# Kernel tuning notes

Hardware: AMD Instinct MI355X
Metric: run time of the kernel (lower is better)

Reference implementation:

```python
import jax, jax.numpy as jnp
import numpy as np

# dims
B, L, HID = 2, 1024, 2048
NH, HD, NKV = 32, 64, 8
INTER = 8192
DSSM, MH, MP, MS, MG, MK = 2048, 32, 64, 64, 1, 4
CONV_DIM = DSSM + 2 * MG * MS
EPS = 1e-5
ROPE_BASE = 1e11
# multipliers from config
KEY_MULT, ATTN_IN, ATTN_OUT = 0.7, 1.2, 0.8
SSM_IN, SSM_OUT = 1.1, 0.9
GATE_MULT, DOWN_MULT = 0.9, 0.8
SSM_MULTS = (1.0, 0.9, 0.8, 1.1, 1.2)


def _rms(x, w, eps=EPS):
    return x * jax.lax.rsqrt(jnp.mean(x * x, -1, keepdims=True) + eps) * w


def _rope(pos, x):  # neox-style, full head_dim; x: (B,L,H,HD)
    half = HD // 2
    inv = ROPE_BASE ** (-jnp.arange(0, HD, 2, dtype=jnp.float32) / HD)
    ang = pos.astype(jnp.float32)[:, None] * inv  # (L, half)
    cos = jnp.cos(ang)[None, :, None, :]
    sin = jnp.sin(ang)[None, :, None, :]
    x1, x2 = x[..., :half], x[..., half:]
    return jnp.concatenate([x1 * cos - x2 * sin, x2 * cos + x1 * sin], -1)


def _mup_vector():
    return jnp.concatenate([
        jnp.full((DSSM,), SSM_MULTS[0], jnp.float32),
        jnp.full((DSSM,), SSM_MULTS[1], jnp.float32),
        jnp.full((MG * MS,), SSM_MULTS[2], jnp.float32),
        jnp.full((MG * MS,), SSM_MULTS[3], jnp.float32),
        jnp.full((MH,), SSM_MULTS[4], jnp.float32),
    ])


def setup_inputs() -> dict:
    key = jax.random.key(0)
    ks = jax.random.split(key, 16)
    s = 0.02
    return {
        "hidden_states": jax.random.normal(ks[0], (B, L, HID), jnp.float32),
        "positions": jnp.arange(L, dtype=jnp.int32),
        "w_in_ln": jnp.ones((HID,), jnp.float32),
        "qkv_w": jax.random.normal(ks[1], (NH * HD + 2 * NKV * HD, HID), jnp.float32) * s,
        "o_w": jax.random.normal(ks[2], (HID, NH * HD), jnp.float32) * s,
        "in_proj_w": jax.random.normal(ks[3], (2 * DSSM + 2 * MG * MS + MH, HID), jnp.float32) * s,
        "conv_w": jax.random.normal(ks[4], (CONV_DIM, MK), jnp.float32) * 0.1,
        "conv_b": jax.random.normal(ks[5], (CONV_DIM,), jnp.float32) * 0.01,
        "A_log": jnp.log(jnp.linspace(1.0, 16.0, MH, dtype=jnp.float32)),
        "dt_bias": jax.random.normal(ks[6], (MH,), jnp.float32) * 0.1,
        "D": jnp.ones((MH,), jnp.float32),
        "ssm_norm_w": jnp.ones((DSSM,), jnp.float32),
        "out_proj_w": jax.random.normal(ks[7], (HID, DSSM), jnp.float32) * s,
        "w_pre_ff_ln": jnp.ones((HID,), jnp.float32),
        "gate_up_w": jax.random.normal(ks[8], (2 * INTER, HID), jnp.float32) * s,
        "down_w": jax.random.normal(ks[9], (HID, INTER), jnp.float32) * s,
    }


def _attention(hs, positions, qkv_w, o_w):
    qkv = hs @ qkv_w.T
    qs, kvs = NH * HD, NKV * HD
    q = qkv[..., :qs].reshape(B, L, NH, HD)
    k = qkv[..., qs:qs + kvs].reshape(B, L, NKV, HD) * KEY_MULT
    v = qkv[..., qs + kvs:].reshape(B, L, NKV, HD)
    q = _rope(positions, q)
    k = _rope(positions, k)
    rep = NH // NKV
    qg = q.reshape(B, L, NKV, rep, HD)
    scores = jnp.einsum('blgrd,bmgd->bgrlm', qg, k) * (HD ** -0.5)
    mask = jnp.tril(jnp.ones((L, L), bool))
    scores = jnp.where(mask[None, None, None], scores, jnp.float32(-1e9))
    attn = jax.nn.softmax(scores, axis=-1)
    out = jnp.einsum('bgrlm,bmgd->blgrd', attn, v).reshape(B, L, NH * HD)
    return out @ o_w.T


def _mamba(hs, in_proj_w, conv_w, conv_b, A_log, dt_bias, D, ssm_norm_w, out_proj_w):
    proj = (hs @ in_proj_w.T) * _mup_vector()  # (B,L,2*DSSM+2*G*S+MH)
    z = proj[..., :DSSM]
    xBC = proj[..., DSSM:DSSM + CONV_DIM]
    dt = proj[..., -MH:]
    # causal depthwise conv1d, kernel MK, then silu
    xpad = jnp.pad(xBC, ((0, 0), (MK - 1, 0), (0, 0)))
    conv = sum(xpad[:, k:k + L, :] * conv_w[:, k] for k in range(MK)) + conv_b
    xBC = jax.nn.silu(conv)
    x = xBC[..., :DSSM].reshape(B, L, MH, MP)
    Bm = xBC[..., DSSM:DSSM + MG * MS].reshape(B, L, MS)  # G=1
    C = xBC[..., DSSM + MG * MS:].reshape(B, L, MS)
    dt = jax.nn.softplus(dt + dt_bias)  # (B,L,MH)
    A = -jnp.exp(A_log)  # (MH,)

    def step(state, inp):  # state: (B,MH,MP,MS)
        x_t, dt_t, b_t, c_t = inp  # (B,MH,MP),(B,MH),(B,MS),(B,MS)
        dA = jnp.exp(dt_t * A)  # (B,MH)
        dBx = dt_t[..., None, None] * x_t[..., None] * b_t[:, None, None, :]
        state = state * dA[..., None, None] + dBx
        y = jnp.einsum('bhps,bs->bhp', state, c_t)
        return state, y

    xs = (jnp.moveaxis(x, 1, 0), jnp.moveaxis(dt, 1, 0),
          jnp.moveaxis(Bm, 1, 0), jnp.moveaxis(C, 1, 0))
    state0 = jnp.zeros((B, MH, MP, MS), hs.dtype)
    _, ys = jax.lax.scan(step, state0, xs)
    y = jnp.moveaxis(ys, 0, 1) + x * D[None, None, :, None]  # (B,L,MH,MP)
    y = y.reshape(B, L, DSSM)
    # gated RMSNorm: gate with silu(z), then rms-normalize
    g = y * jax.nn.silu(z)
    g = _rms(g, ssm_norm_w)
    return g @ out_proj_w.T


def _mlp(x, gate_up_w, down_w):
    gu = x @ gate_up_w.T
    gate = gu[..., :INTER] * GATE_MULT
    up = gu[..., INTER:]
    return (jax.nn.silu(gate) * up) @ down_w.T * DOWN_MULT


def reference(hidden_states, positions, w_in_ln, qkv_w, o_w, in_proj_w, conv_w,
              conv_b, A_log, dt_bias, D, ssm_norm_w, out_proj_w, w_pre_ff_ln,
              gate_up_w, down_w):
    residual = hidden_states
    hs = _rms(hidden_states, w_in_ln)
    attn_h = _attention(hs * ATTN_IN, positions, qkv_w, o_w)
    ssm_h = _mamba(hs * SSM_IN, in_proj_w, conv_w, conv_b, A_log, dt_bias, D,
                   ssm_norm_w, out_proj_w)
    h = attn_h * ATTN_OUT + ssm_h * SSM_OUT + residual
    residual = h
    h = _rms(h, w_pre_ff_ln)
    h = _mlp(h, gate_up_w, down_w)
    return h + residual
```

## Files before the change

### kernel.cpp

```cpp
#include <hip/hip_runtime.h>
#include <hip/hip_bf16.h>
#include <math.h>

#define B_      2
#define L_      1024
#define HID     2048
#define T_      (B_*L_)
#define NH      32
#define HD      64
#define NKV     8
#define INTER   8192
#define DSSM    2048
#define MH      32
#define MP      64
#define MS      64
#define MK      4
#define CONV_DIM 2176
#define QKV_N   3072
#define INPROJ_N 4256
#define CH      16
#define CL      64

typedef __bf16 bf16x8 __attribute__((ext_vector_type(8)));
typedef __bf16 bf16x4 __attribute__((ext_vector_type(4)));
typedef float  floatx4 __attribute__((ext_vector_type(4)));

static const size_t OFF_H2   = 0;
static const size_t OFF_MUP  = 4194304;
static const size_t AR       = 4210688;
static const size_t OFF_WQKV = AR;
static const size_t OFF_WIN  = OFF_WQKV + 3145728;
static const size_t OFF_WO   = OFF_WIN  + 4358144;
static const size_t OFF_WOP  = OFF_WO   + 2097152;
static const size_t OFF_HSB  = OFF_WOP  + 2097152;
static const size_t OFF_HSF  = OFF_HSB  + 2097152;
static const size_t OFF_QKV  = OFF_HSF  + 4194304;
static const size_t OFF_Q    = OFF_QKV  + 6291456;
static const size_t OFF_K    = OFF_Q    + 2097152;
static const size_t OFF_V    = OFF_K    + 524288;
static const size_t OFF_ATT  = OFF_V    + 524288;
static const size_t OFF_PROJ = OFF_ATT  + 2097152;
static const size_t OFF_XBC  = OFF_PROJ + 8716288;
static const size_t OFF_Y    = OFF_XBC  + 4456448;
static const size_t OFF_G    = OFF_Y    + 4194304;
static const size_t OFF_TB   = OFF_QKV;
static const size_t OFF_DEC  = OFF_Q;
static const size_t OFF_LAM  = OFF_V;
static const size_t OFF_HS2B = AR;
static const size_t OFF_GU   = AR + 2097152;
static const size_t OFF_ACTB = OFF_GU + 33554432;
static const size_t OFF_WB2  = OFF_ACTB + 8388608;

__device__ inline float block_sum(float v, float* red) {
#pragma unroll
  for (int o = 32; o > 0; o >>= 1) v += __shfl_down(v, o, 64);
  const int lane = threadIdx.x & 63, wv = threadIdx.x >> 6;
  if (lane == 0) red[wv] = v;
  __syncthreads();
  if (threadIdx.x == 0) red[0] = red[0] + red[1] + red[2] + red[3];
  __syncthreads();
  float r = red[0];
  __syncthreads();
  return r;
}

__device__ inline bf16x8 pack8(float4 a, float4 b, float scale) {
  bf16x8 v;
  v[0] = (__bf16)(a.x * scale); v[1] = (__bf16)(a.y * scale);
  v[2] = (__bf16)(a.z * scale); v[3] = (__bf16)(a.w * scale);
  v[4] = (__bf16)(b.x * scale); v[5] = (__bf16)(b.y * scale);
  v[6] = (__bf16)(b.z * scale); v[7] = (__bf16)(b.w * scale);
  return v;
}

__device__ __forceinline__ void async16(const void* g, void* l) {
  __builtin_amdgcn_global_load_lds(
      (const __attribute__((address_space(1))) void*)g,
      (__attribute__((address_space(3))) void*)l, 16, 0, 0);
}

__global__ __launch_bounds__(256) void cvt_kernel(
    const float* __restrict__ in, __bf16* __restrict__ outp, int n8)
{
  int i = blockIdx.x * 256 + threadIdx.x;
  const int stride = gridDim.x * 256;
  for (; i < n8; i += stride) {
    const float4* p = (const float4*)(in + (size_t)i * 8);
    float4 a = p[0], b = p[1];
    bf16x8 v;
    v[0] = (__bf16)a.x; v[1] = (__bf16)a.y; v[2] = (__bf16)a.z; v[3] = (__bf16)a.w;
    v[4] = (__bf16)b.x; v[5] = (__bf16)b.y; v[6] = (__bf16)b.z; v[7] = (__bf16)b.w;
    *(bf16x8*)(outp + (size_t)i * 8) = v;
  }
}

__global__ __launch_bounds__(256) void copy_kernel(
    const float* __restrict__ in, float* __restrict__ outp)
{
  const size_t i = ((size_t)blockIdx.x * 256 + threadIdx.x) * 4;
  *(float4*)&outp[i] = *(const float4*)&in[i];
}

__global__ __launch_bounds__(256) void gemm_bf_kernel(
    const __bf16* __restrict__ A, const __bf16* __restrict__ W,
    float* __restrict__ out, const float* __restrict__ addin,
    const float* __restrict__ colscale,
    int N, int K, int ldo, float alpha)
{
  __shared__ __align__(16) __bf16 As[2][128 * 32];
  __shared__ __align__(16) __bf16 Bs[2][128 * 32];
  const int tid = threadIdx.x;
  const int lane = tid & 63, wave = tid >> 6;
  const int fr = lane & 15, fq = lane >> 4;

  const int nwg = (int)(gridDim.x * gridDim.y);
  int lid = (int)(blockIdx.y * gridDim.x + blockIdx.x);
  lid = (lid & 7) * (nwg >> 3) + (lid >> 3);
  const int m0 = (lid & 15) * 128;
  const int n0 = (lid >> 4) * 128;
  const int wm = (wave >> 1) * 64, wn = (wave & 1) * 64;

  const int KS = K / gridDim.z;
  const int kbase = (int)blockIdx.z * KS;

  const int srow = wave * 32 + (lane >> 2);
  const int selem = (lane & 3) * 8;
  const __bf16* ga0 = A + (size_t)(m0 + srow) * K + kbase + selem;
  const __bf16* ga1 = ga0 + (size_t)16 * K;
  int wr0 = n0 + srow;      if (wr0 >= N) wr0 = N - 1;
  int wr1 = n0 + srow + 16; if (wr1 >= N) wr1 = N - 1;
  const __bf16* gb0 = W + (size_t)wr0 * K + kbase + selem;
  const __bf16* gb1 = W + (size_t)wr1 * K + kbase + selem;
  const int sbase = wave * 2 * 512;

  floatx4 acc[4][4];
#pragma unroll
  for (int i = 0; i < 4; i++)
#pragma unroll
    for (int j = 0; j < 4; j++) acc[i][j] = (floatx4){0.f, 0.f, 0.f, 0.f};

  async16(ga0, &As[0][sbase]); async16(ga1, &As[0][sbase + 512]);
  async16(gb0, &Bs[0][sbase]); async16(gb1, &Bs[0][sbase + 512]);
  ga0 += 32; ga1 += 32; gb0 += 32; gb1 += 32;
  __syncthreads();

  const int nsteps = KS >> 5;
  int cur = 0;
  for (int s = 0; s < nsteps - 1; ++s) {
    async16(ga0, &As[cur ^ 1][sbase]); async16(ga1, &As[cur ^ 1][sbase + 512]);
    async16(gb0, &Bs[cur ^ 1][sbase]); async16(gb1, &Bs[cur ^ 1][sbase + 512]);
    ga0 += 32; ga1 += 32; gb0 += 32; gb1 += 32;

    bf16x8 aF[4], bF[4];
#pragma unroll
    for (int i = 0; i < 4; i++)
      aF[i] = *(const bf16x8*)&As[cur][(wm + i * 16 + fr) * 32 + fq * 8];
#pragma unroll
    for (int j = 0; j < 4; j++)
      bF[j] = *(const bf16x8*)&Bs[cur][(wn + j * 16 + fr) * 32 + fq * 8];
#pragma unroll
    for (int i = 0; i < 4; i++)
#pragma unroll
      for (int j = 0; j < 4; j++)
        acc[i][j] = __builtin_amdgcn_mfma_f32_16x16x32_bf16(aF[i], bF[j], acc[i][j], 0, 0, 0);

    __syncthreads();
    cur ^= 1;
  }

  {
    bf16x8 aF[4], bF[4];
#pragma unroll
    for (int i = 0; i < 4; i++)
      aF[i] = *(const bf16x8*)&As[cur][(wm + i * 16 + fr) * 32 + fq * 8];
#pragma unroll
    for (int j = 0; j < 4; j++)
      bF[j] = *(const bf16x8*)&Bs[cur][(wn + j * 16 + fr) * 32 + fq * 8];
#pragma unroll
    for (int i = 0; i < 4; i++)
#pragma unroll
      for (int j = 0; j < 4; j++)
        acc[i][j] = __builtin_amdgcn_mfma_f32_16x16x32_bf16(aF[i], bF[j], acc[i][j], 0, 0, 0);
  }

  const bool at = (gridDim.z > 1);
#pragma unroll
  for (int i = 0; i < 4; i++) {
#pragma unroll
    for (int r = 0; r < 4; r++) {
      const int m = m0 + wm + i * 16 + fq * 4 + r;
      float* orow = out + (size_t)m * ldo;
      const float* arow = addin ? (addin + (size_t)m * ldo) : nullptr;
#pragma unroll
      for (int j = 0; j < 4; j++) {
        const int n = n0 + wn + j * 16 + fr;
        if (n < N) {
          float vv = acc[i][j][r] * alpha;
          if (colscale) vv *= colscale[n];
          if (at) {
            atomicAdd(&orow[n], vv);
          } else {
            if (arow) vv += arow[n];
            orow[n] = vv;
          }
        }
      }
    }
  }
}

__global__ __launch_bounds__(256) void rms_kernel(
    const float* __restrict__ in, const float* __restrict__ w,
    __bf16* __restrict__ outb, float* __restrict__ outf, float* __restrict__ copy)
{
  __shared__ float buf[HID];
  __shared__ float red[8];
  const int tid = threadIdx.x;
  const size_t t = blockIdx.x;
  const float* row = in + t * HID;
  float ss = 0.f;
  for (int i = tid; i < HID; i += 256) { float x = row[i]; buf[i] = x; ss += x * x; }
  float tot = block_sum(ss, red);
  float inv = rsqrtf(tot / (float)HID + 1e-5f);
  for (int i = tid; i < HID; i += 256) {
    float x = buf[i];
    float val = x * inv * w[i];
    outb[t * HID + i] = (__bf16)val;
    if (outf) outf[t * HID + i] = val;
    if (copy) copy[t * HID + i] = x;
  }
}

__global__ void mup_kernel(float* __restrict__ mup) {
  int i = blockIdx.x * 256 + threadIdx.x;
  if (i >= INPROJ_N) return;
  float v = (i < DSSM) ? 1.0f
          : (i < 2 * DSSM) ? 0.9f
          : (i < 2 * DSSM + MS) ? 0.8f
          : (i < 2 * DSSM + 2 * MS) ? 1.1f
          : 1.2f;
  mup[i] = v;
}

__global__ __launch_bounds__(256) void rope_kernel(
    const float* __restrict__ qkv, const int* __restrict__ positions,
    __bf16* __restrict__ q, __bf16* __restrict__ k, __bf16* __restrict__ v)
{
  __shared__ float inv_s[32];
  const int tid = threadIdx.x;
  const size_t t = blockIdx.x;
  const int l = (int)(t & (L_ - 1));
  if (tid < 32) inv_s[tid] = powf(1.0e11f, -(float)(2 * tid) / 64.f);
  __syncthreads();
  const float pos = (float)positions[l];
  const float* src = qkv + t * QKV_N;
  for (int idx = tid; idx < 1536; idx += 256) {
    int head = idx >> 5, hd = idx & 31;
    if (head < 32) {
      float ang = pos * inv_s[hd];
      float c = cosf(ang), sn = sinf(ang);
      float x1 = src[head * 64 + hd], x2 = src[head * 64 + 32 + hd];
      __bf16* dst = q + (t * NH + head) * HD;
      dst[hd] = (__bf16)((x1 * c - x2 * sn) * 0.125f);
      dst[hd + 32] = (__bf16)((x2 * c + x1 * sn) * 0.125f);
    } else if (head < 40) {
      int kk = head - 32;
      float ang = pos * inv_s[hd];
      float c = cosf(ang), sn = sinf(ang);
      float x1 = src[2048 + kk * 64 + hd] * 0.7f;
      float x2 = src[2048 + kk * 64 + 32 + hd] * 0.7f;
      __bf16* dst = k + (t * NKV + kk) * HD;
      dst[hd] = (__bf16)(x1 * c - x2 * sn);
      dst[hd + 32] = (__bf16)(x2 * c + x1 * sn);
    } else {
      int vv = head - 40;
      __bf16* dst = v + (t * NKV + vv) * HD;
      dst[hd] = (__bf16)src[2560 + vv * 64 + hd];
      dst[hd + 32] = (__bf16)src[2560 + vv * 64 + 32 + hd];
    }
  }
}

__global__ __launch_bounds__(256) void fattn_kernel(
    const __bf16* __restrict__ q, const __bf16* __restrict__ k,
    const __bf16* __restrict__ v, __bf16* __restrict__ out)
{
  __shared__ __align__(16) __bf16 Vt[64][72];
  __shared__ __align__(16) __bf16 Ps[4][16][72];
  const int tid = threadIdx.x;
  const int wave = tid >> 6, lane = tid & 63;
  const int fr = lane & 15, fq = lane >> 4;
  const int qt = (int)(gridDim.x - 1) - blockIdx.x;
  const int h = blockIdx.y, b = blockIdx.z, g = h >> 2;
  const int l0 = qt * 64;

  bf16x8 qf[2];
  {
    const int qrow = l0 + wave * 16 + fr;
    const __bf16* qp = q + (((size_t)(b * L_ + qrow)) * NH + h) * HD;
    qf[0] = *(const bf16x8*)&qp[fq * 8];
    qf[1] = *(const bf16x8*)&qp[32 + fq * 8];
  }

  floatx4 O[4];
  float m_run[4], l_run[4];
#pragma unroll
  for (int i = 0; i < 4; i++) { O[i] = (floatx4){0.f,0.f,0.f,0.f}; m_run[i] = -3.0e38f; l_run[i] = 0.f; }

  for (int kt = 0; kt <= qt; kt++) {
    __syncthreads();
#pragma unroll
    for (int pp = 0; pp < 4; pp++) {
      const int kb = pp * 4 + wave;
      bf16x4 pk;
#pragma unroll
      for (int c = 0; c < 4; c++)
        pk[c] = v[(((size_t)(b * L_ + kt * 64 + kb * 4 + c)) * NKV + g) * HD + lane];
      *(bf16x4*)&Vt[lane][kb * 4] = pk;
    }

    floatx4 S[4];
#pragma unroll
    for (int j = 0; j < 4; j++) {
      const __bf16* kp = k + (((size_t)(b * L_ + kt * 64 + j * 16 + fr)) * NKV + g) * HD;
      floatx4 sa = (floatx4){0.f,0.f,0.f,0.f};
#pragma unroll
      for (int s = 0; s < 2; s++) {
        bf16x8 kf = *(const bf16x8*)&kp[s * 32 + fq * 8];
        sa = __builtin_amdgcn_mfma_f32_16x16x32_bf16(qf[s], kf, sa, 0, 0, 0);
      }
      S[j] = sa;
    }

    if (kt == qt) {
      const int qbase = wave * 16 + fq * 4;
#pragma unroll
      for (int j = 0; j < 4; j++)
#pragma unroll
        for (int r = 0; r < 4; r++)
          if (j * 16 + fr > qbase + r) S[j][r] = -1.0e30f;
    }

    float rm[4], alpha[4], rsum[4];
#pragma unroll
    for (int r = 0; r < 4; r++)
      rm[r] = fmaxf(fmaxf(S[0][r], S[1][r]), fmaxf(S[2][r], S[3][r]));
#pragma unroll
    for (int msk = 1; msk <= 8; msk <<= 1)
#pragma unroll
      for (int r = 0; r < 4; r++) rm[r] = fmaxf(rm[r], __shfl_xor(rm[r], msk, 64));
#pragma unroll
    for (int r = 0; r < 4; r++) {
      float mnew = fmaxf(m_run[r], rm[r]);
      alpha[r] = __expf(m_run[r] - mnew);
      m_run[r] = mnew;
    }
#pragma unroll
    for (int j = 0; j < 4; j++)
#pragma unroll
      for (int r = 0; r < 4; r++) S[j][r] = __expf(S[j][r] - m_run[r]);
#pragma unroll
    for (int r = 0; r < 4; r++)
      rsum[r] = S[0][r] + S[1][r] + S[2][r] + S[3][r];
#pragma unroll
    for (int msk = 1; msk <= 8; msk <<= 1)
#pragma unroll
      for (int r = 0; r < 4; r++) rsum[r] += __shfl_xor(rsum[r], msk, 64);
#pragma unroll
    for (int r = 0; r < 4; r++) l_run[r] = l_run[r] * alpha[r] + rsum[r];
#pragma unroll
    for (int d4 = 0; d4 < 4; d4++)
#pragma unroll
      for (int r = 0; r < 4; r++) O[d4][r] *= alpha[r];

#pragma unroll
    for (int j = 0; j < 4; j++)
#pragma unroll
      for (int r = 0; r < 4; r++)
        Ps[wave][fq * 4 + r][j * 16 + fr] = (__bf16)S[j][r];

    __syncthreads();

#pragma unroll
    for (int s = 0; s < 2; s++) {
      bf16x8 pf = *(const bf16x8*)&Ps[wave][fr][s * 32 + fq * 8];
#pragma unroll
      for (int d4 = 0; d4 < 4; d4++) {
        bf16x8 vf = *(const bf16x8*)&Vt[d4 * 16 + fr][s * 32 + fq * 8];
        O[d4] = __builtin_amdgcn_mfma_f32_16x16x32_bf16(pf, vf, O[d4], 0, 0, 0);
      }
    }
  }

  float rl[4];
#pragma unroll
  for (int r = 0; r < 4; r++) rl[r] = 1.f / l_run[r];
#pragma unroll
  for (int d4 = 0; d4 < 4; d4++)
#pragma unroll
    for (int r = 0; r < 4; r++) {
      const int qg = l0 + wave * 16 + fq * 4 + r;
      out[((size_t)(b * L_ + qg)) * HID + h * 64 + d4 * 16 + fr] = (__bf16)(O[d4][r] * rl[r]);
    }
}

__global__ __launch_bounds__(256) void dtfix_kernel(
    const float* __restrict__ hs_ln, const float* __restrict__ w, float* __restrict__ proj)
{
  const size_t t = blockIdx.x;
  const int tid = threadIdx.x;
  const int o = tid >> 3, part = tid & 7;
  const float* a = hs_ln + t * HID;
  const float* wr = w + (size_t)(INPROJ_N - MH + o) * HID;
  float s = 0.f;
  for (int kk = part * 4; kk < HID; kk += 32) {
    const float4 av = *(const float4*)&a[kk];
    const float4 wv = *(const float4*)&wr[kk];
    s += av.x * wv.x + av.y * wv.y + av.z * wv.z + av.w * wv.w;
  }
  s += __shfl_xor(s, 1);
  s += __shfl_xor(s, 2);
  s += __shfl_xor(s, 4);
  if (part == 0) proj[t * INPROJ_N + (INPROJ_N - MH) + o] = s * 1.32f;
}

__global__ __launch_bounds__(256) void conv_kernel(
    const float* __restrict__ proj, const float* __restrict__ cw,
    const float* __restrict__ cb, float* __restrict__ xbc)
{
  const int c = blockIdx.x * 256 + threadIdx.x;
  if (c >= CONV_DIM) return;
  const int t = blockIdx.y;
  const int l = t & (L_ - 1);
  float acc = cb[c];
#pragma unroll
  for (int kk = 0; kk < MK; kk++) {
    int lp = l - (MK - 1) + kk;
    if (lp >= 0)
      acc += proj[((size_t)(t - (MK - 1) + kk)) * INPROJ_N + DSSM + c] * cw[c * MK + kk];
  }
  xbc[(size_t)t * CONV_DIM + c] = acc / (1.f + __expf(-acc));
}

__global__ __launch_bounds__(256) void scanA_kernel(
    const float* __restrict__ xbc, const float* __restrict__ proj,
    const float* __restrict__ A_log, const float* __restrict__ dt_bias,
    const float* __restrict__ Dp,
    float* __restrict__ y, float* __restrict__ Tbuf,
    float* __restrict__ lam, float* __restrict__ dec)
{
  __shared__ __align__(16) __bf16 xT[64][72];
  __shared__ __align__(16) __bf16 BTw[64][72];
  __shared__ __align__(16) __bf16 Braw[64][72];
  __shared__ __align__(16) __bf16 Craw[64][72];
  __shared__ __align__(16) __bf16 Ps[4][16][72];
  __shared__ float dt_s[64], cum_s[64];

  const int tid = threadIdx.x;
  const int lane = tid & 63, wave = tid >> 6;
  const int fr = lane & 15, fq = lane >> 4;
  const int c = blockIdx.x, h = blockIdx.y, b = blockIdx.z;
  const int t0 = b * L_ + c * CL;
  const float Ah = -expf(A_log[h]);
  const float dtb = dt_bias[h], Dh = Dp[h];

  if (wave == 0) {
    float draw = proj[(size_t)(t0 + lane) * INPROJ_N + (INPROJ_N - MH) + h];
    float dtv = draw + dtb;
    dtv = (dtv > 20.f) ? dtv : log1pf(__expf(dtv));
    float cs = dtv * Ah;
#pragma unroll
    for (int d = 1; d < 64; d <<= 1) {
      float nv = __shfl_up(cs, d, 64);
      if (lane >= d) cs += nv;
    }
    dt_s[lane] = dtv;
    cum_s[lane] = cs;
  }

#pragma unroll
  for (int pass = 0; pass < 4; pass++) {
    const int l = pass * 16 + (tid >> 4);
    const int s4 = (tid & 15) * 4;
    const float* rowp = xbc + (size_t)(t0 + l) * CONV_DIM;
    float4 xv = *(const float4*)&rowp[h * 64 + s4];
    float4 bv = *(const float4*)&rowp[DSSM + s4];
    float4 cv = *(const float4*)&rowp[DSSM + MS + s4];
    xT[s4 + 0][l] = (__bf16)xv.x;
    xT[s4 + 1][l] = (__bf16)xv.y;
    xT[s4 + 2][l] = (__bf16)xv.z;
    xT[s4 + 3][l] = (__bf16)xv.w;
    bf16x4 b4; b4[0]=(__bf16)bv.x; b4[1]=(__bf16)bv.y; b4[2]=(__bf16)bv.z; b4[3]=(__bf16)bv.w;
    *(bf16x4*)&Braw[l][s4] = b4;
    bf16x4 c4; c4[0]=(__bf16)cv.x; c4[1]=(__bf16)cv.y; c4[2]=(__bf16)cv.z; c4[3]=(__bf16)cv.w;
    *(bf16x4*)&Craw[l][s4] = c4;
  }
  __syncthreads();

  const float cend = cum_s[63];
#pragma unroll
  for (int pass = 0; pass < 4; pass++) {
    const int l = pass * 16 + (tid >> 4);
    const int s4 = (tid & 15) * 4;
    const float wl = __expf(cend - cum_s[l]) * dt_s[l];
    float4 bv = *(const float4*)&xbc[(size_t)(t0 + l) * CONV_DIM + DSSM + s4];
    BTw[s4 + 0][l] = (__bf16)(bv.x * wl);
    BTw[s4 + 1][l] = (__bf16)(bv.y * wl);
    BTw[s4 + 2][l] = (__bf16)(bv.z * wl);
    BTw[s4 + 3][l] = (__bf16)(bv.w * wl);
  }

  {
    bf16x8 aF0 = *(const bf16x8*)&Craw[wave * 16 + fr][fq * 8];
    bf16x8 aF1 = *(const bf16x8*)&Craw[wave * 16 + fr][fq * 8 + 32];
#pragma unroll
    for (int j = 0; j < 4; j++) {
      floatx4 s = (floatx4){0.f,0.f,0.f,0.f};
      bf16x8 b0 = *(const bf16x8*)&Braw[j * 16 + fr][fq * 8];
      bf16x8 b1 = *(const bf16x8*)&Braw[j * 16 + fr][fq * 8 + 32];
      s = __builtin_amdgcn_mfma_f32_16x16x32_bf16(aF0, b0, s, 0, 0, 0);
      s = __builtin_amdgcn_mfma_f32_16x16x32_bf16(aF1, b1, s, 0, 0, 0);
      const int m = j * 16 + fr;
      const float dtm = dt_s[m], cmm = cum_s[m];
#pragma unroll
      for (int r = 0; r < 4; r++) {
        const int lR = wave * 16 + fq * 4 + r;
        float f = (m <= lR) ? __expf(cum_s[lR] - cmm) * dtm : 0.f;
        Ps[wave][fq * 4 + r][m] = (__bf16)(s[r] * f);
      }
    }
  }
  __syncthreads();

  {
    bf16x8 aF0 = *(const bf16x8*)&Ps[wave][fr][fq * 8];
    bf16x8 aF1 = *(const bf16x8*)&Ps[wave][fr][fq * 8 + 32];
#pragma unroll
    for (int j = 0; j < 4; j++) {
      floatx4 s = (floatx4){0.f,0.f,0.f,0.f};
      bf16x8 b0 = *(const bf16x8*)&xT[j * 16 + fr][fq * 8];
      bf16x8 b1 = *(const bf16x8*)&xT[j * 16 + fr][fq * 8 + 32];
      s = __builtin_amdgcn_mfma_f32_16x16x32_bf16(aF0, b0, s, 0, 0, 0);
      s = __builtin_amdgcn_mfma_f32_16x16x32_bf16(aF1, b1, s, 0, 0, 0);
      const int p = j * 16 + fr;
#pragma unroll
      for (int r = 0; r < 4; r++) {
        const int lR = wave * 16 + fq * 4 + r;
        float xval = (float)xT[p][lR];
        y[(size_t)(t0 + lR) * DSSM + h * 64 + p] = s[r] + Dh * xval;
      }
    }
  }

  {
    float* Tb = Tbuf + ((size_t)((b * MH + h) * CH + c)) * 4096;
    bf16x8 aF0 = *(const bf16x8*)&xT[wave * 16 + fr][fq * 8];
    bf16x8 aF1 = *(const bf16x8*)&xT[wave * 16 + fr][fq * 8 + 32];
#pragma unroll
    for (int j = 0; j < 4; j++) {
      floatx4 s = (floatx4){0.f,0.f,0.f,0.f};
      bf16x8 b0 = *(const bf16x8*)&BTw[j * 16 + fr][fq * 8];
      bf16x8 b1 = *(const bf16x8*)&BTw[j * 16 + fr][fq * 8 + 32];
      s = __builtin_amdgcn_mfma_f32_16x16x32_bf16(aF0, b0, s, 0, 0, 0);
      s = __builtin_amdgcn_mfma_f32_16x16x32_bf16(aF1, b1, s, 0, 0, 0);
#pragma unroll
      for (int r = 0; r < 4; r++)
        Tb[(wave * 16 + fq * 4 + r) * 64 + j * 16 + fr] = s[r];
    }
  }

  if (tid == 0) lam[(b * MH + h) * CH + c] = __expf(cend);
  if (tid >= 64 && tid < 128)
    dec[((size_t)((b * MH + h) * CH + c)) * 64 + (tid - 64)] = __expf(cum_s[tid - 64]);
}

__global__ __launch_bounds__(256) void scanB_kernel(
    const float* __restrict__ xbc, const float* __restrict__ Tbuf,
    const float* __restrict__ lam, const float* __restrict__ dec,
    float* __restrict__ y)
{
  __shared__ __align__(16) float S[64][68];
  __shared__ __align__(16) __bf16 Cc[64][72];
  __shared__ float decl[64];
  const int tid = threadIdx.x;
  const int lane = tid & 63, wave = tid >> 6;
  const int fr = lane & 15, fq = lane >> 4;
  const int h = blockIdx.x, b = blockIdx.y;

  const int sown = tid & 63, pbase = (tid >> 6) * 16;
#pragma unroll
  for (int i = 0; i < 16; i++) S[pbase + i][sown] = 0.f;
  __syncthreads();

  for (int c = 0; c < CH; c++) {
    const int t0 = b * L_ + c * CL;
#pragma unroll
    for (int pass = 0; pass < 4; pass++) {
      const int l = pass * 16 + (tid >> 4);
      const int s4 = (tid & 15) * 4;
      float4 cv = *(const float4*)&xbc[(size_t)(t0 + l) * CONV_DIM + DSSM + MS + s4];
      bf16x4 c4; c4[0]=(__bf16)cv.x; c4[1]=(__bf16)cv.y; c4[2]=(__bf16)cv.z; c4[3]=(__bf16)cv.w;
      *(bf16x4*)&Cc[l][s4] = c4;
    }
    if (tid < 64) decl[tid] = dec[((size_t)((b * MH + h) * CH + c)) * 64 + tid];
    __syncthreads();

    if (c > 0) {
      bf16x8 aF0 = *(const bf16x8*)&Cc[wave * 16 + fr][fq * 8];
      bf16x8 aF1 = *(const bf16x8*)&Cc[wave * 16 + fr][fq * 8 + 32];
#pragma unroll
      for (int j = 0; j < 4; j++) {
        const float* srow = &S[j * 16 + fr][0];
        float4 s0 = *(const float4*)&srow[fq * 8];
        float4 s1 = *(const float4*)&srow[fq * 8 + 4];
        float4 s2 = *(const float4*)&srow[fq * 8 + 32];
        float4 s3 = *(const float4*)&srow[fq * 8 + 36];
        bf16x8 b0 = pack8(s0, s1, 1.f);
        bf16x8 b1 = pack8(s2, s3, 1.f);
        floatx4 acc = (floatx4){0.f,0.f,0.f,0.f};
        acc = __builtin_amdgcn_mfma_f32_16x16x32_bf16(aF0, b0, acc, 0, 0, 0);
        acc = __builtin_amdgcn_mfma_f32_16x16x32_bf16(aF1, b1, acc, 0, 0, 0);
        const int p = j * 16 + fr;
#pragma unroll
        for (int r = 0; r < 4; r++) {
          const int lR = wave * 16 + fq * 4 + r;
          float* yp = &y[(size_t)(t0 + lR) * DSSM + h * 64 + p];
          *yp += decl[lR] * acc[r];
        }
      }
    }
    __syncthreads();

    const float lc = lam[(b * MH + h) * CH + c];
    const float* Tb = Tbuf + ((size_t)((b * MH + h) * CH + c)) * 4096;
#pragma unroll
    for (int i = 0; i < 16; i++) {
      float tv = Tb[(pbase + i) * 64 + sown];
      S[pbase + i][sown] = lc * S[pbase + i][sown] + tv;
    }
    __syncthreads();
  }
}

__global__ __launch_bounds__(256) void gating_kernel(
    const float* __restrict__ y, const float* __restrict__ proj,
    const float* __restrict__ nw, __bf16* __restrict__ g)
{
  __shared__ float buf[DSSM];
  __shared__ float red[8];
  const int tid = threadIdx.x;
  const size_t t = blockIdx.x;
  float ss = 0.f;
  for (int i = tid; i < DSSM; i += 256) {
    float zv = proj[t * INPROJ_N + i];
    float yv = y[t * DSSM + i];
    float gv = yv * zv / (1.f + __expf(-zv));
    buf[i] = gv;
    ss += gv * gv;
  }
  float tot = block_sum(ss, red);
  float inv = rsqrtf(tot / (float)DSSM + 1e-5f);
  for (int i = tid; i < DSSM; i += 256) g[t * DSSM + i] = (__bf16)(buf[i] * inv * nw[i]);
}

__global__ __launch_bounds__(256) void act_kernel(
    const float* __restrict__ gu, __bf16* __restrict__ act)
{
  const int i = (blockIdx.x * 256 + threadIdx.x) * 4;
  const size_t t = blockIdx.y;
  float4 g4 = *(const float4*)&gu[t * (2 * INTER) + i];
  float4 u4 = *(const float4*)&gu[t * (2 * INTER) + INTER + i];
  bf16x4 o;
  float gt;
  gt = g4.x * 0.9f; o[0] = (__bf16)(gt / (1.f + __expf(-gt)) * u4.x);
  gt = g4.y * 0.9f; o[1] = (__bf16)(gt / (1.f + __expf(-gt)) * u4.y);
  gt = g4.z * 0.9f; o[2] = (__bf16)(gt / (1.f + __expf(-gt)) * u4.z);
  gt = g4.w * 0.9f; o[3] = (__bf16)(gt / (1.f + __expf(-gt)) * u4.w);
  *(bf16x4*)&act[t * INTER + i] = o;
}

extern "C" void kernel_launch(void* const* d_in, const int* in_sizes, int n_in,
                              void* d_out, int out_size, void* d_ws, size_t ws_size,
                              hipStream_t stream)
{
  const float* hidden      = (const float*)d_in[0];
  const int*   positions   = (const int*)d_in[1];
  const float* w_in_ln     = (const float*)d_in[2];
  const float* qkv_w       = (const float*)d_in[3];
  const float* o_w         = (const float*)d_in[4];
  const float* in_proj_w   = (const float*)d_in[5];
  const float* conv_w      = (const float*)d_in[6];
  const float* conv_b      = (const float*)d_in[7];
  const float* A_log       = (const float*)d_in[8];
  const float* dt_bias     = (const float*)d_in[9];
  const float* Dp          = (const float*)d_in[10];
  const float* ssm_norm_w  = (const float*)d_in[11];
  const float* out_proj_w  = (const float*)d_in[12];
  const float* w_pre_ff_ln = (const float*)d_in[13];
  const float* gate_up_w   = (const float*)d_in[14];
  const float* down_w      = (const float*)d_in[15];
  (void)in_sizes; (void)n_in; (void)out_size; (void)ws_size;

  float* ws   = (float*)d_ws;
  float* outp = (float*)d_out;

  float*  h2    = ws + OFF_H2;
  float*  mup   = ws + OFF_MUP;
  __bf16* wqkv  = (__bf16*)(ws + OFF_WQKV);
  __bf16* win   = (__bf16*)(ws + OFF_WIN);
  __bf16* wo    = (__bf16*)(ws + OFF_WO);
  __bf16* wop   = (__bf16*)(ws + OFF_WOP);
  __bf16* hsb   = (__bf16*)(ws + OFF_HSB);
  float*  hsf   = ws + OFF_HSF;
  float*  qkv   = ws + OFF_QKV;
  __bf16* qb    = (__bf16*)(ws + OFF_Q);
  __bf16* kb    = (__bf16*)(ws + OFF_K);
  __bf16* vb    = (__bf16*)(ws + OFF_V);
  __bf16* attb  = (__bf16*)(ws + OFF_ATT);
  float*  proj  = ws + OFF_PROJ;
  float*  xbc   = ws + OFF_XBC;
  float*  y     = ws + OFF_Y;
  __bf16* gb    = (__bf16*)(ws + OFF_G);
  float*  Tbuf  = ws + OFF_TB;
  float*  dec   = ws + OFF_DEC;
  float*  lam   = ws + OFF_LAM;
  __bf16* hs2b  = (__bf16*)(ws + OFF_HS2B);
  float*  gu    = ws + OFF_GU;
  __bf16* actb  = (__bf16*)(ws + OFF_ACTB);
  __bf16* wb2   = (__bf16*)(ws + OFF_WB2);

  cvt_kernel<<<2048, 256, 0, stream>>>(qkv_w, wqkv, 786432);
  cvt_kernel<<<2048, 256, 0, stream>>>(in_proj_w, win, 1089536);
  cvt_kernel<<<2048, 256, 0, stream>>>(o_w, wo, 524288);
  cvt_kernel<<<2048, 256, 0, stream>>>(out_proj_w, wop, 524288);
  mup_kernel<<<17, 256, 0, stream>>>(mup);
  rms_kernel<<<T_, 256, 0, stream>>>(hidden, w_in_ln, hsb, hsf, h2);

  gemm_bf_kernel<<<dim3(16, 24, 1), 256, 0, stream>>>(hsb, wqkv, qkv, nullptr, nullptr,
                                                      QKV_N, HID, QKV_N, 1.2f);
  rope_kernel<<<T_, 256, 0, stream>>>(qkv, positions, qb, kb, vb);
  fattn_kernel<<<dim3(L_ / 64, NH, B_), 256, 0, stream>>>(qb, kb, vb, attb);
  gemm_bf_kernel<<<dim3(16, 16, 4), 256, 0, stream>>>(attb, wo, h2, nullptr, nullptr,
                                                      HID, HID, HID, 0.8f);

  gemm_bf_kernel<<<dim3(16, 34, 1), 256, 0, stream>>>(hsb, win, proj, nullptr, mup,
                                                      INPROJ_N, HID, INPROJ_N, 1.1f);
  dtfix_kernel<<<T_, 256, 0, stream>>>(hsf, in_proj_w, proj);
  conv_kernel<<<dim3(9, T_), 256, 0, stream>>>(proj, conv_w, conv_b, xbc);
  scanA_kernel<<<dim3(CH, MH, B_), 256, 0, stream>>>(xbc, proj, A_log, dt_bias, Dp,
                                                     y, Tbuf, lam, dec);
  scanB_kernel<<<dim3(MH, B_), 256, 0, stream>>>(xbc, Tbuf, lam, dec, y);
  gating_kernel<<<T_, 256, 0, stream>>>(y, proj, ssm_norm_w, gb);
  gemm_bf_kernel<<<dim3(16, 16, 4), 256, 0, stream>>>(gb, wop, h2, nullptr, nullptr,
                                                      HID, HID, HID, 0.9f);

  rms_kernel<<<T_, 256, 0, stream>>>(h2, w_pre_ff_ln, hs2b, nullptr, nullptr);
  cvt_kernel<<<2048, 256, 0, stream>>>(gate_up_w, wb2, 2097152);
  gemm_bf_kernel<<<dim3(16, 64, 1), 256, 0, stream>>>(hs2b, wb2, gu, nullptr, nullptr,
                                                      INTER, HID, 2 * INTER, 1.0f);
  cvt_kernel<<<2048, 256, 0, stream>>>(gate_up_w + (size_t)INTER * HID, wb2, 2097152);
  gemm_bf_kernel<<<dim3(16, 64, 1), 256, 0, stream>>>(hs2b, wb2, gu + INTER, nullptr, nullptr,
                                                      INTER, HID, 2 * INTER, 1.0f);
  act_kernel<<<dim3(INTER / 1024, T_), 256, 0, stream>>>(gu, actb);
  cvt_kernel<<<2048, 256, 0, stream>>>(down_w, wb2, 2097152);
  copy_kernel<<<4096, 256, 0, stream>>>(h2, outp);
  gemm_bf_kernel<<<dim3(16, 16, 4), 256, 0, stream>>>(actb, wb2, outp, nullptr, nullptr,
                                                      HID, INTER, HID, 0.8f);
}
```

Before: 1.265 ms.

## Add 256x256-tile bf16 GEMM kernel for large projections and MLP

```diff
diff --git a/kernel.cpp b/kernel.cpp
--- a/kernel.cpp
+++ b/kernel.cpp
@@ -103,8 +103,7 @@
 
 __global__ __launch_bounds__(256) void gemm_bf_kernel(
     const __bf16* __restrict__ A, const __bf16* __restrict__ W,
-    float* __restrict__ out, const float* __restrict__ addin,
-    const float* __restrict__ colscale,
+    float* __restrict__ out, const float* __restrict__ colscale,
     int N, int K, int ldo, float alpha)
 {
   __shared__ __align__(16) __bf16 As[2][128 * 32];
@@ -146,11 +145,12 @@
 
   const int nsteps = KS >> 5;
   int cur = 0;
-  for (int s = 0; s < nsteps - 1; ++s) {
-    async16(ga0, &As[cur ^ 1][sbase]); async16(ga1, &As[cur ^ 1][sbase + 512]);
-    async16(gb0, &Bs[cur ^ 1][sbase]); async16(gb1, &Bs[cur ^ 1][sbase + 512]);
-    ga0 += 32; ga1 += 32; gb0 += 32; gb1 += 32;
-
+  for (int s = 0; s < nsteps; ++s) {
+    if (s + 1 < nsteps) {
+      async16(ga0, &As[cur ^ 1][sbase]); async16(ga1, &As[cur ^ 1][sbase + 512]);
+      async16(gb0, &Bs[cur ^ 1][sbase]); async16(gb1, &Bs[cur ^ 1][sbase + 512]);
+      ga0 += 32; ga1 += 32; gb0 += 32; gb1 += 32;
+    }
     bf16x8 aF[4], bF[4];
 #pragma unroll
     for (int i = 0; i < 4; i++)
@@ -163,24 +163,8 @@
 #pragma unroll
       for (int j = 0; j < 4; j++)
         acc[i][j] = __builtin_amdgcn_mfma_f32_16x16x32_bf16(aF[i], bF[j], acc[i][j], 0, 0, 0);
-
     __syncthreads();
     cur ^= 1;
-  }
-
-  {
-    bf16x8 aF[4], bF[4];
-#pragma unroll
-    for (int i = 0; i < 4; i++)
-      aF[i] = *(const bf16x8*)&As[cur][(wm + i * 16 + fr) * 32 + fq * 8];
-#pragma unroll
-    for (int j = 0; j < 4; j++)
-      bF[j] = *(const bf16x8*)&Bs[cur][(wn + j * 16 + fr) * 32 + fq * 8];
-#pragma unroll
-    for (int i = 0; i < 4; i++)
-#pragma unroll
-      for (int j = 0; j < 4; j++)
-        acc[i][j] = __builtin_amdgcn_mfma_f32_16x16x32_bf16(aF[i], bF[j], acc[i][j], 0, 0, 0);
   }
 
   const bool at = (gridDim.z > 1);
@@ -190,19 +174,112 @@
     for (int r = 0; r < 4; r++) {
       const int m = m0 + wm + i * 16 + fq * 4 + r;
       float* orow = out + (size_t)m * ldo;
-      const float* arow = addin ? (addin + (size_t)m * ldo) : nullptr;
 #pragma unroll
       for (int j = 0; j < 4; j++) {
         const int n = n0 + wn + j * 16 + fr;
         if (n < N) {
           float vv = acc[i][j][r] * alpha;
           if (colscale) vv *= colscale[n];
-          if (at) {
-            atomicAdd(&orow[n], vv);
-          } else {
-            if (arow) vv += arow[n];
-            orow[n] = vv;
-          }
+          if (at) atomicAdd(&orow[n], vv);
+          else    orow[n] = vv;
+        }
+      }
+    }
+  }
+}
+
+__global__ __launch_bounds__(512, 2) void gemm256_kernel(
+    const __bf16* __restrict__ A, const __bf16* __restrict__ W,
+    float* __restrict__ out, int N, int K, int ldo, float alpha)
+{
+  __shared__ __align__(16) __bf16 As[2][256 * 64];
+  __shared__ __align__(16) __bf16 Bs[2][256 * 64];
+  const int tid = threadIdx.x;
+  const int lane = tid & 63, wave = tid >> 6;
+  const int fr = lane & 15, fq = lane >> 4;
+
+  const int nwg = (int)(gridDim.x * gridDim.y);
+  int lid = (int)(blockIdx.y * gridDim.x + blockIdx.x);
+  lid = (lid & 7) * (nwg >> 3) + (lid >> 3);
+  const int m0 = (lid & 7) * 256;
+  const int n0 = (lid >> 3) * 256;
+  const int wm = (wave >> 2) * 128;
+  const int wn = (wave & 3) * 64;
+
+  const int KS = K / gridDim.z;
+  const int kbase = (int)blockIdx.z * KS;
+
+  const int strow = wave * 8 + (lane >> 3);
+  const int stcol = (lane & 7) * 8;
+  const __bf16* gA = A + (size_t)(m0 + strow) * K + kbase + stcol;
+  const __bf16* gB[4];
+#pragma unroll
+  for (int q = 0; q < 4; q++) {
+    int nr = n0 + q * 64 + strow;
+    if (nr >= N) nr = N - 1;
+    gB[q] = W + (size_t)nr * K + kbase + stcol;
+  }
+  const int sdst = wave * 512;
+
+  floatx4 acc[8][4];
+#pragma unroll
+  for (int i = 0; i < 8; i++)
+#pragma unroll
+    for (int j = 0; j < 4; j++) acc[i][j] = (floatx4){0.f, 0.f, 0.f, 0.f};
+
+#pragma unroll
+  for (int q = 0; q < 4; q++) {
+    async16(gA + (size_t)q * 64 * K, &As[0][q * 4096 + sdst]);
+    async16(gB[q],                   &Bs[0][q * 4096 + sdst]);
+  }
+  __syncthreads();
+
+  const int nsteps = KS >> 6;
+  int cur = 0;
+  for (int s = 0; s < nsteps; ++s) {
+    if (s + 1 < nsteps) {
+      const int ko = (s + 1) * 64;
+#pragma unroll
+      for (int q = 0; q < 4; q++) {
+        async16(gA + ko + (size_t)q * 64 * K, &As[cur ^ 1][q * 4096 + sdst]);
+        async16(gB[q] + ko,                   &Bs[cur ^ 1][q * 4096 + sdst]);
+      }
+    }
+
+    bf16x8 bF[4][2];
+#pragma unroll
+    for (int j = 0; j < 4; j++)
+#pragma unroll
+      for (int t = 0; t < 2; t++)
+        bF[j][t] = *(const bf16x8*)&Bs[cur][(wn + j * 16 + fr) * 64 + t * 32 + fq * 8];
+#pragma unroll
+    for (int i = 0; i < 8; i++) {
+      bf16x8 a0 = *(const bf16x8*)&As[cur][(wm + i * 16 + fr) * 64 + fq * 8];
+      bf16x8 a1 = *(const bf16x8*)&As[cur][(wm + i * 16 + fr) * 64 + 32 + fq * 8];
+#pragma unroll
+      for (int j = 0; j < 4; j++) {
+        acc[i][j] = __builtin_amdgcn_mfma_f32_16x16x32_bf16(a0, bF[j][0], acc[i][j], 0, 0, 0);
+        acc[i][j] = __builtin_amdgcn_mfma_f32_16x16x32_bf16(a1, bF[j][1], acc[i][j], 0, 0, 0);
+      }
+    }
+    __syncthreads();
+    cur ^= 1;
+  }
+
+  const bool at = (gridDim.z > 1);
+#pragma unroll
+  for (int i = 0; i < 8; i++) {
+#pragma unroll
+    for (int r = 0; r < 4; r++) {
+      const int m = m0 + wm + i * 16 + fq * 4 + r;
+      float* orow = out + (size_t)m * ldo;
+#pragma unroll
+      for (int j = 0; j < 4; j++) {
+        const int n = n0 + wn + j * 16 + fr;
+        if (n < N) {
+          float vv = acc[i][j][r] * alpha;
+          if (at) atomicAdd(&orow[n], vv);
+          else    orow[n] = vv;
         }
       }
     }
@@ -736,14 +813,14 @@
   mup_kernel<<<17, 256, 0, stream>>>(mup);
   rms_kernel<<<T_, 256, 0, stream>>>(hidden, w_in_ln, hsb, hsf, h2);
 
-  gemm_bf_kernel<<<dim3(16, 24, 1), 256, 0, stream>>>(hsb, wqkv, qkv, nullptr, nullptr,
+  gemm_bf_kernel<<<dim3(16, 24, 1), 256, 0, stream>>>(hsb, wqkv, qkv, nullptr,
                                                       QKV_N, HID, QKV_N, 1.2f);
   rope_kernel<<<T_, 256, 0, stream>>>(qkv, positions, qb, kb, vb);
   fattn_kernel<<<dim3(L_ / 64, NH, B_), 256, 0, stream>>>(qb, kb, vb, attb);
-  gemm_bf_kernel<<<dim3(16, 16, 4), 256, 0, stream>>>(attb, wo, h2, nullptr, nullptr,
-                                                      HID, HID, HID, 0.8f);
-
-  gemm_bf_kernel<<<dim3(16, 34, 1), 256, 0, stream>>>(hsb, win, proj, nullptr, mup,
+  gemm256_kernel<<<dim3(8, 8, 4), 512, 0, stream>>>(attb, wo, h2,
+                                                    HID, HID, HID, 0.8f);
+
+  gemm_bf_kernel<<<dim3(16, 34, 1), 256, 0, stream>>>(hsb, win, proj, mup,
                                                       INPROJ_N, HID, INPROJ_N, 1.1f);
   dtfix_kernel<<<T_, 256, 0, stream>>>(hsf, in_proj_w, proj);
   conv_kernel<<<dim3(9, T_), 256, 0, stream>>>(proj, conv_w, conv_b, xbc);
@@ -751,19 +828,19 @@
                                                      y, Tbuf, lam, dec);
   scanB_kernel<<<dim3(MH, B_), 256, 0, stream>>>(xbc, Tbuf, lam, dec, y);
   gating_kernel<<<T_, 256, 0, stream>>>(y, proj, ssm_norm_w, gb);
-  gemm_bf_kernel<<<dim3(16, 16, 4), 256, 0, stream>>>(gb, wop, h2, nullptr, nullptr,
-                                                      HID, HID, HID, 0.9f);
+  gemm256_kernel<<<dim3(8, 8, 4), 512, 0, stream>>>(gb, wop, h2,
+                                                    HID, HID, HID, 0.9f);
 
   rms_kernel<<<T_, 256, 0, stream>>>(h2, w_pre_ff_ln, hs2b, nullptr, nullptr);
   cvt_kernel<<<2048, 256, 0, stream>>>(gate_up_w, wb2, 2097152);
-  gemm_bf_kernel<<<dim3(16, 64, 1), 256, 0, stream>>>(hs2b, wb2, gu, nullptr, nullptr,
-                                                      INTER, HID, 2 * INTER, 1.0f);
+  gemm256_kernel<<<dim3(8, 32, 1), 512, 0, stream>>>(hs2b, wb2, gu,
+                                                     INTER, HID, 2 * INTER, 1.0f);
   cvt_kernel<<<2048, 256, 0, stream>>>(gate_up_w + (size_t)INTER * HID, wb2, 2097152);
-  gemm_bf_kernel<<<dim3(16, 64, 1), 256, 0, stream>>>(hs2b, wb2, gu + INTER, nullptr, nullptr,
-                                                      INTER, HID, 2 * INTER, 1.0f);
+  gemm256_kernel<<<dim3(8, 32, 1), 512, 0, stream>>>(hs2b, wb2, gu + INTER,
+                                                     INTER, HID, 2 * INTER, 1.0f);
   act_kernel<<<dim3(INTER / 1024, T_), 256, 0, stream>>>(gu, actb);
   cvt_kernel<<<2048, 256, 0, stream>>>(down_w, wb2, 2097152);
   copy_kernel<<<4096, 256, 0, stream>>>(h2, outp);
-  gemm_bf_kernel<<<dim3(16, 16, 4), 256, 0, stream>>>(actb, wb2, outp, nullptr, nullptr,
-                                                      HID, INTER, HID, 0.8f);
-}
+  gemm256_kernel<<<dim3(8, 8, 4), 512, 0, stream>>>(actb, wb2, outp,
+                                                    HID, INTER, HID, 0.8f);
+}
```

New measurement: 1.191 ms. -5.8%, faster.
